# Kernel tuning notes

Hardware: AMD Instinct MI355X
Metric: run time of the kernel (lower is better)

Reference implementation:

```python
import jax, jax.numpy as jnp
import numpy as np

DT_RANK = 128
DIM_INNER = 2048
D_STATE = 16
IN_FEATURES = 2048


def setup_inputs() -> dict:
    key = jax.random.key(0)
    ks = jax.random.split(key, 6)
    B, L = 2, 2048
    x = jax.random.normal(ks[0], (B, L, IN_FEATURES), dtype=jnp.float32)
    out_dbc = DT_RANK + 2 * D_STATE
    W_dbc = jax.random.normal(ks[1], (out_dbc, IN_FEATURES), dtype=jnp.float32) / np.sqrt(IN_FEATURES)
    b_dbc = jax.random.normal(ks[2], (out_dbc,), dtype=jnp.float32) * 0.01
    W_dt = jax.random.normal(ks[3], (DIM_INNER, DT_RANK), dtype=jnp.float32) / np.sqrt(DT_RANK)
    b_dt = jax.random.normal(ks[4], (DIM_INNER,), dtype=jnp.float32) * 0.01
    A_log = jnp.log(jnp.tile(jnp.arange(1, D_STATE + 1, dtype=jnp.float32), (DIM_INNER, 1)))
    D = jnp.ones((DIM_INNER,), dtype=jnp.float32)
    return {"x": x, "W_dbc": W_dbc, "b_dbc": b_dbc, "W_dt": W_dt, "b_dt": b_dt, "A_log": A_log, "D": D}


def _scan_combine(e1, e2):
    a1, b1 = e1
    a2, b2 = e2
    return a1 * a2, a2 * b1 + b2


def reference(x, W_dbc, b_dbc, W_dt, b_dt, A_log, D):
    # x: (B, L, Din) with Din == dim_inner
    A = -jnp.exp(A_log)                               # (Din, N)
    deltaBC = x @ W_dbc.T + b_dbc                     # (B, L, dt_rank + 2N)
    delta_lo = deltaBC[..., :DT_RANK]
    Bmat = deltaBC[..., DT_RANK:DT_RANK + D_STATE]    # (B, L, N)
    Cmat = deltaBC[..., DT_RANK + D_STATE:]           # (B, L, N)
    delta = jax.nn.softplus(delta_lo @ W_dt.T + b_dt) # (B, L, Din)
    deltaA = jnp.exp(delta[..., None] * A)            # (B, L, Din, N)
    BX = (delta[..., None] * Bmat[:, :, None, :]) * x[..., None]  # (B, L, Din, N)
    # first-order linear recurrence h_t = deltaA_t * h_{t-1} + BX_t, h_{-1}=0
    _, hs = jax.lax.associative_scan(_scan_combine, (deltaA, BX), axis=1)
    y = jnp.einsum("blds,bls->bld", hs, Cmat) + D * x
    return y
```

## Files before the change

kernel.cpp:

```cpp
#include <hip/hip_runtime.h>
#include <hip/hip_bf16.h>
#include <math.h>

#define BATCH  2
#define LSEQ   2048
#define FEAT   2048
#define DINNER 2048
#define DSTATE 16
#define DTRANK 128
#define NDBC   160
#define NCHUNK 64
#define LCHUNK (LSEQ / NCHUNK)
#define BL     (BATCH * LSEQ)
#define KSPLIT 4
#define KCH    (FEAT / KSPLIT)
#define KSUB   64
#define BSTRIDE 72

typedef __attribute__((ext_vector_type(8))) short bf16x8;
typedef __attribute__((ext_vector_type(4))) short bf16x4;
typedef __attribute__((ext_vector_type(4))) float floatx4;

#if __has_builtin(__builtin_amdgcn_exp2f)
#define EXP2F(x) __builtin_amdgcn_exp2f(x)
#else
#define EXP2F(x) exp2f(x)
#endif
#if __has_builtin(__builtin_amdgcn_logf)
#define LOG2F(x) __builtin_amdgcn_logf(x)
#else
#define LOG2F(x) __log2f(x)
#endif

__device__ inline float softplus_fast(float v) {
    float e = EXP2F(-fabsf(v) * 1.4426950408889634f);
    return fmaxf(v, 0.f) + 0.6931471805599453f * LOG2F(1.f + e);
}

__device__ inline void split8(floatx4 a0, floatx4 a1, bf16x8* h, bf16x8* l) {
    union { bf16x8 v; __hip_bfloat16 e[8]; } H, L;
    float v[8] = {a0[0], a0[1], a0[2], a0[3], a1[0], a1[1], a1[2], a1[3]};
#pragma unroll
    for (int i = 0; i < 8; ++i) {
        H.e[i] = __float2bfloat16(v[i]);
        L.e[i] = __float2bfloat16(v[i] - __bfloat162float(H.e[i]));
    }
    *h = H.v; *l = L.v;
}

__device__ inline void split_store8(const float* __restrict__ src, int t,
                                    __hip_bfloat16* __restrict__ hi,
                                    __hip_bfloat16* __restrict__ lo) {
    const floatx4* s4 = (const floatx4*)(src) + t * 2;
    bf16x8 h, l;
    split8(s4[0], s4[1], &h, &l);
    ((bf16x8*)hi)[t] = h;
    ((bf16x8*)lo)[t] = l;
}

__global__ __launch_bounds__(256) void prep_all(
    const float* __restrict__ Wdbc, const float* __restrict__ Wdt,
    const float* __restrict__ Alog,
    __hip_bfloat16* __restrict__ wdbch, __hip_bfloat16* __restrict__ wdbcl,
    __hip_bfloat16* __restrict__ wdth, __hip_bfloat16* __restrict__ wdtl,
    float* __restrict__ A2T)
{
    int blk = blockIdx.x;
    if (blk < 160) {
        split_store8(Wdbc, blk * 256 + threadIdx.x, wdbch, wdbcl);
    } else if (blk < 288) {
        split_store8(Wdt, (blk - 160) * 256 + threadIdx.x, wdth, wdtl);
    } else {
        int tid = (blk - 288) * 256 + threadIdx.x;
        int s = tid >> 11;
        int d = tid & (DINNER - 1);
        A2T[s * DINNER + d] = -__expf(Alog[d * DSTATE + s]) * 1.4426950408889634f;
    }
}

__global__ __launch_bounds__(256) void gemm_dbc(
    const float* __restrict__ x,
    const __hip_bfloat16* __restrict__ wh, const __hip_bfloat16* __restrict__ wl,
    float* __restrict__ partial)
{
    __shared__ union {
        struct { __hip_bfloat16 Bh[NDBC * BSTRIDE]; __hip_bfloat16 Bl[NDBC * BSTRIDE]; } s;
        float tile[64 * 164];
    } sm;
    int mt = blockIdx.x, ks = blockIdx.y;
    int t = threadIdx.x;
    int wave = t >> 6, lane = t & 63, lm = lane & 15, q = lane >> 4;
    int m0 = mt * 64;
    int k0 = ks * KCH;
    const float* xrow = x + (size_t)(m0 + wave * 16 + lm) * FEAT;
    floatx4 acc[10];
#pragma unroll
    for (int i = 0; i < 10; ++i) acc[i] = (floatx4){0.f, 0.f, 0.f, 0.f};
    int sr = t >> 3, scb = t & 7;
    for (int kc = 0; kc < KCH; kc += KSUB) {
#pragma unroll
        for (int r = sr; r < NDBC; r += 32) {
            size_t g = (size_t)r * FEAT + k0 + kc + scb * 8;
            *(bf16x8*)&sm.s.Bh[r * BSTRIDE + scb * 8] = *(const bf16x8*)&wh[g];
            *(bf16x8*)&sm.s.Bl[r * BSTRIDE + scb * 8] = *(const bf16x8*)&wl[g];
        }
        __syncthreads();
#pragma unroll
        for (int kk = 0; kk < KSUB; kk += 32) {
            int col = k0 + kc + kk + q * 8;
            floatx4 a0 = *(const floatx4*)(xrow + col);
            floatx4 a1 = *(const floatx4*)(xrow + col + 4);
            bf16x8 ah, al;
            split8(a0, a1, &ah, &al);
#pragma unroll
            for (int nt = 0; nt < 10; ++nt) {
                int boff = (nt * 16 + lm) * BSTRIDE + kk + q * 8;
                bf16x8 bh = *(const bf16x8*)&sm.s.Bh[boff];
                bf16x8 bl = *(const bf16x8*)&sm.s.Bl[boff];
                acc[nt] = __builtin_amdgcn_mfma_f32_16x16x32_bf16(ah, bh, acc[nt], 0, 0, 0);
                acc[nt] = __builtin_amdgcn_mfma_f32_16x16x32_bf16(ah, bl, acc[nt], 0, 0, 0);
                acc[nt] = __builtin_amdgcn_mfma_f32_16x16x32_bf16(al, bh, acc[nt], 0, 0, 0);
            }
        }
        __syncthreads();
    }
#pragma unroll
    for (int nt = 0; nt < 10; ++nt)
#pragma unroll
        for (int i = 0; i < 4; ++i)
            sm.tile[(wave * 16 + q * 4 + i) * 164 + nt * 16 + lm] = acc[nt][i];
    __syncthreads();
#pragma unroll
    for (int it = 0; it < 10; ++it) {
        int idx = it * 256 + t;
        int row = idx / 40, cq = (idx - row * 40) * 4;
        floatx4 v = *(const floatx4*)&sm.tile[row * 164 + cq];
        *(floatx4*)&partial[((size_t)ks * BL + m0 + row) * NDBC + cq] = v;
    }
}

__global__ __launch_bounds__(256) void finalize_dbc(
    const float* __restrict__ partial, const float* __restrict__ bias,
    float* __restrict__ dbcBC, __hip_bfloat16* __restrict__ dhi, __hip_bfloat16* __restrict__ dlo)
{
    int tid = blockIdx.x * 256 + threadIdx.x;
    int m = tid / 40, c4 = tid - m * 40;
    int n = c4 * 4;
    floatx4 s = *(const floatx4*)(bias + n);
#pragma unroll
    for (int ks = 0; ks < KSPLIT; ++ks) {
        floatx4 p = *(const floatx4*)(partial + ((size_t)ks * BL + m) * NDBC + n);
        s = s + p;
    }
    if (c4 < 32) {
        union { bf16x4 v; __hip_bfloat16 e[4]; } H, L;
#pragma unroll
        for (int i = 0; i < 4; ++i) {
            H.e[i] = __float2bfloat16(s[i]);
            L.e[i] = __float2bfloat16(s[i] - __bfloat162float(H.e[i]));
        }
        *(bf16x4*)(dhi + (size_t)m * DTRANK + n) = H.v;
        *(bf16x4*)(dlo + (size_t)m * DTRANK + n) = L.v;
    } else {
        *(floatx4*)(dbcBC + (size_t)m * 32 + (n - 128)) = s;
    }
}

__global__ __launch_bounds__(256) void gemm_dt(
    const __hip_bfloat16* __restrict__ dhi, const __hip_bfloat16* __restrict__ dlo,
    const __hip_bfloat16* __restrict__ wh, const __hip_bfloat16* __restrict__ wl,
    const float* __restrict__ bdt, float* __restrict__ delta)
{
    __shared__ float tile[128 * 68];
    int mt = blockIdx.x, ntb = blockIdx.y;
    int t = threadIdx.x, wave = t >> 6, lane = t & 63, lm = lane & 15, q = lane >> 4;
    int m0 = mt * 128 + wave * 32;
    int n0 = ntb * 64;
    bf16x8 AH[2][4], AL[2][4];
#pragma unroll
    for (int sub = 0; sub < 2; ++sub) {
        const __hip_bfloat16* ah = dhi + (size_t)(m0 + sub * 16 + lm) * DTRANK + q * 8;
        const __hip_bfloat16* al = dlo + (size_t)(m0 + sub * 16 + lm) * DTRANK + q * 8;
#pragma unroll
        for (int kp = 0; kp < 4; ++kp) {
            AH[sub][kp] = *(const bf16x8*)(ah + kp * 32);
            AL[sub][kp] = *(const bf16x8*)(al + kp * 32);
        }
    }
    floatx4 acc[4][2];
#pragma unroll
    for (int i = 0; i < 4; ++i)
#pragma unroll
        for (int j = 0; j < 2; ++j) acc[i][j] = (floatx4){0.f, 0.f, 0.f, 0.f};
#pragma unroll
    for (int nt = 0; nt < 4; ++nt) {
        const __hip_bfloat16* bh = wh + (size_t)(n0 + nt * 16 + lm) * DTRANK + q * 8;
        const __hip_bfloat16* blp = wl + (size_t)(n0 + nt * 16 + lm) * DTRANK + q * 8;
#pragma unroll
        for (int kp = 0; kp < 4; ++kp) {
            bf16x8 bhv = *(const bf16x8*)(bh + kp * 32);
            bf16x8 blv = *(const bf16x8*)(blp + kp * 32);
#pragma unroll
            for (int sub = 0; sub < 2; ++sub) {
                acc[nt][sub] = __builtin_amdgcn_mfma_f32_16x16x32_bf16(AH[sub][kp], bhv, acc[nt][sub], 0, 0, 0);
                acc[nt][sub] = __builtin_amdgcn_mfma_f32_16x16x32_bf16(AH[sub][kp], blv, acc[nt][sub], 0, 0, 0);
                acc[nt][sub] = __builtin_amdgcn_mfma_f32_16x16x32_bf16(AL[sub][kp], bhv, acc[nt][sub], 0, 0, 0);
            }
        }
    }
    int wrow = wave * 32;
#pragma unroll
    for (int nt = 0; nt < 4; ++nt) {
        float bias = bdt[n0 + nt * 16 + lm];
#pragma unroll
        for (int sub = 0; sub < 2; ++sub)
#pragma unroll
            for (int i = 0; i < 4; ++i) {
                float v = acc[nt][sub][i] + bias;
                tile[(wrow + sub * 16 + q * 4 + i) * 68 + nt * 16 + lm] = softplus_fast(v);
            }
    }
    __syncthreads();
#pragma unroll
    for (int it = 0; it < 8; ++it) {
        int idx = it * 256 + t;
        int row = idx >> 4, cq = (idx & 15) * 4;
        floatx4 v = *(const floatx4*)&tile[row * 68 + cq];
        *(floatx4*)&delta[(size_t)(mt * 128 + row) * DINNER + n0 + cq] = v;
    }
}

__global__ __launch_bounds__(256) void scan_partial(
    const float* __restrict__ delta, const float* __restrict__ x,
    const float* __restrict__ dbcBC, const float* __restrict__ A2T,
    float* __restrict__ hA, float* __restrict__ sumd)
{
    __shared__ float BC[LCHUNK * 32];
    int t = threadIdx.x;
    int gtid = blockIdx.x * 256 + t;
    int d = gtid & (DINNER - 1);
    int c = (gtid >> 11) & (NCHUNK - 1);
    int b = gtid >> 17;
    {
        int row = t >> 3, cq = (t & 7) * 4;
        *(floatx4*)&BC[row * 32 + cq] =
            *(const floatx4*)&dbcBC[(size_t)(b * LSEQ + c * LCHUNK + row) * 32 + cq];
    }
    float a2[DSTATE], h[DSTATE];
#pragma unroll
    for (int s = 0; s < DSTATE; ++s) { a2[s] = A2T[s * DINNER + d]; h[s] = 0.f; }
    __syncthreads();
    int base = (b * LSEQ + c * LCHUNK) * DINNER + d;
    const float* dp = delta + base;
    const float* xp = x + base;
    float sd = 0.f;
    auto step = [&](int i, float dl, float xv) {
        float du = dl * xv;
        sd += dl;
        const floatx4* Bq = (const floatx4*)&BC[i * 32];
#pragma unroll
        for (int qq = 0; qq < 4; ++qq) {
            floatx4 Bv = Bq[qq];
#pragma unroll
            for (int j = 0; j < 4; ++j) {
                int s = qq * 4 + j;
                h[s] = fmaf(EXP2F(dl * a2[s]), h[s], du * Bv[j]);
            }
        }
    };
    float dlA = dp[0], xvA = xp[0];
    float dlB = dp[DINNER], xvB = xp[DINNER];
    for (int i = 0; i < LCHUNK - 2; ++i) {
        float dlC = dp[(i + 2) * DINNER];
        float xvC = xp[(i + 2) * DINNER];
        step(i, dlA, xvA);
        dlA = dlB; xvA = xvB; dlB = dlC; xvB = xvC;
    }
    step(LCHUNK - 2, dlA, xvA);
    step(LCHUNK - 1, dlB, xvB);
    size_t hbase = ((size_t)((b * NCHUNK + c) * 4) * DINNER + d) * 4;
#pragma unroll
    for (int qq = 0; qq < 4; ++qq) {
        floatx4 v = {h[qq * 4], h[qq * 4 + 1], h[qq * 4 + 2], h[qq * 4 + 3]};
        *(floatx4*)&hA[hbase + (size_t)qq * DINNER * 4] = v;
    }
    sumd[(size_t)(b * NCHUNK + c) * DINNER + d] = sd;
}

__global__ __launch_bounds__(256) void scan_combine(
    float* __restrict__ hA, const float* __restrict__ sumd, const float* __restrict__ A2T)
{
    int tid = blockIdx.x * 256 + threadIdx.x;
    int s = tid & 15;
    int d = (tid >> 4) & (DINNER - 1);
    int b = tid >> 15;
    float a2s = A2T[s * DINNER + d];
    int q = s >> 2, e = s & 3;
    size_t hoff = ((size_t)(b * NCHUNK * 4 + q) * DINNER + d) * 4 + e;
    size_t soff = (size_t)(b * NCHUNK) * DINNER + d;
    const size_t hstep = (size_t)16 * DINNER;
    float hin = 0.f;
#pragma unroll
    for (int g = 0; g < NCHUNK / 16; ++g) {
        float sdv[16], hv[16];
#pragma unroll
        for (int k = 0; k < 16; ++k) {
            int cc = g * 16 + k;
            sdv[k] = sumd[soff + (size_t)cc * DINNER];
            hv[k] = hA[hoff + (size_t)cc * hstep];
        }
#pragma unroll
        for (int k = 0; k < 16; ++k) {
            int cc = g * 16 + k;
            hA[hoff + (size_t)cc * hstep] = hin;
            hin = EXP2F(a2s * sdv[k]) * hin + hv[k];
        }
    }
}

__global__ __launch_bounds__(256) void scan_final(
    const float* __restrict__ delta, const float* __restrict__ x,
    const float* __restrict__ dbcBC, const float* __restrict__ A2T,
    const float* __restrict__ hin, const float* __restrict__ Dp,
    float* __restrict__ out)
{
    __shared__ float BC[LCHUNK * 32];
    int t = threadIdx.x;
    int gtid = blockIdx.x * 256 + t;
    int d = gtid & (DINNER - 1);
    int c = (gtid >> 11) & (NCHUNK - 1);
    int b = gtid >> 17;
    {
        int row = t >> 3, cq = (t & 7) * 4;
        *(floatx4*)&BC[row * 32 + cq] =
            *(const floatx4*)&dbcBC[(size_t)(b * LSEQ + c * LCHUNK + row) * 32 + cq];
    }
    float a2[DSTATE], h[DSTATE];
    size_t hbase = ((size_t)((b * NCHUNK + c) * 4) * DINNER + d) * 4;
#pragma unroll
    for (int qq = 0; qq < 4; ++qq) {
        floatx4 v = *(const floatx4*)&hin[hbase + (size_t)qq * DINNER * 4];
#pragma unroll
        for (int j = 0; j < 4; ++j) h[qq * 4 + j] = v[j];
    }
#pragma unroll
    for (int s = 0; s < DSTATE; ++s) a2[s] = A2T[s * DINNER + d];
    float Dd = Dp[d];
    __syncthreads();
    int base = (b * LSEQ + c * LCHUNK) * DINNER + d;
    const float* dp = delta + base;
    const float* xp = x + base;
    float* op = out + base;
    auto step = [&](int i, float dl, float xv) {
        float du = dl * xv;
        float y = 0.f;
        const floatx4* Pq = (const floatx4*)&BC[i * 32];
#pragma unroll
        for (int qq = 0; qq < 4; ++qq) {
            floatx4 Bv = Pq[qq];
            floatx4 Cv = Pq[qq + 4];
#pragma unroll
            for (int j = 0; j < 4; ++j) {
                int s = qq * 4 + j;
                h[s] = fmaf(EXP2F(dl * a2[s]), h[s], du * Bv[j]);
                y = fmaf(h[s], Cv[j], y);
            }
        }
        op[i * DINNER] = fmaf(Dd, xv, y);
    };
    float dlA = dp[0], xvA = xp[0];
    float dlB = dp[DINNER], xvB = xp[DINNER];
    for (int i = 0; i < LCHUNK - 2; ++i) {
        float dlC = dp[(i + 2) * DINNER];
        float xvC = xp[(i + 2) * DINNER];
        step(i, dlA, xvA);
        dlA = dlB; xvA = xvB; dlB = dlC; xvB = xvC;
    }
    step(LCHUNK - 2, dlA, xvA);
    step(LCHUNK - 1, dlB, xvB);
}

extern "C" void kernel_launch(void* const* d_in, const int* in_sizes, int n_in,
                              void* d_out, int out_size, void* d_ws, size_t ws_size,
                              hipStream_t stream) {
    const float* x    = (const float*)d_in[0];
    const float* Wdbc = (const float*)d_in[1];
    const float* bdbc = (const float*)d_in[2];
    const float* Wdt  = (const float*)d_in[3];
    const float* bdt  = (const float*)d_in[4];
    const float* Alog = (const float*)d_in[5];
    const float* Dp   = (const float*)d_in[6];
    float* out = (float*)d_out;

    char* w = (char*)d_ws;
    __hip_bfloat16* wdbch = (__hip_bfloat16*)w;  w += (size_t)NDBC * FEAT * 2;
    __hip_bfloat16* wdbcl = (__hip_bfloat16*)w;  w += (size_t)NDBC * FEAT * 2;
    __hip_bfloat16* wdth = (__hip_bfloat16*)w;   w += (size_t)DINNER * DTRANK * 2;
    __hip_bfloat16* wdtl = (__hip_bfloat16*)w;   w += (size_t)DINNER * DTRANK * 2;
    float* partial = (float*)w;                  w += (size_t)KSPLIT * BL * NDBC * 4;
    float* dbcBC = (float*)w;                    w += (size_t)BL * 32 * 4;
    __hip_bfloat16* dhi = (__hip_bfloat16*)w;    w += (size_t)BL * DTRANK * 2;
    __hip_bfloat16* dlo = (__hip_bfloat16*)w;    w += (size_t)BL * DTRANK * 2;
    float* delta = (float*)w;                    w += (size_t)BL * DINNER * 4;
    float* A2T = (float*)w;                      w += (size_t)DSTATE * DINNER * 4;
    float* hA = (float*)w;                       w += (size_t)BATCH * NCHUNK * DINNER * DSTATE * 4;
    float* sumd = (float*)w;                     w += (size_t)BATCH * NCHUNK * DINNER * 4;

    hipLaunchKernelGGL(prep_all, dim3(416), dim3(256), 0, stream,
                       Wdbc, Wdt, Alog, wdbch, wdbcl, wdth, wdtl, A2T);
    hipLaunchKernelGGL(gemm_dbc, dim3(BL / 64, KSPLIT), dim3(256), 0, stream,
                       x, wdbch, wdbcl, partial);
    hipLaunchKernelGGL(finalize_dbc, dim3(BL * 40 / 256), dim3(256), 0, stream,
                       partial, bdbc, dbcBC, dhi, dlo);
    hipLaunchKernelGGL(gemm_dt, dim3(BL / 128, DINNER / 64), dim3(256), 0, stream,
                       dhi, dlo, wdth, wdtl, bdt, delta);
    hipLaunchKernelGGL(scan_partial, dim3((BATCH * NCHUNK * DINNER) / 256), dim3(256), 0, stream,
                       delta, x, dbcBC, A2T, hA, sumd);
    hipLaunchKernelGGL(scan_combine, dim3((BATCH * DINNER * DSTATE) / 256), dim3(256), 0, stream,
                       hA, sumd, A2T);
    hipLaunchKernelGGL(scan_final, dim3((BATCH * NCHUNK * DINNER) / 256), dim3(256), 0, stream,
                       delta, x, dbcBC, A2T, hA, Dp, out);
}
```

Baseline: 210.5 us.

## Batch-prefetch scan inputs in groups of eight and double K-split of projection GEMM

```diff
diff --git a/kernel.cpp b/kernel.cpp
--- a/kernel.cpp
+++ b/kernel.cpp
@@ -12,10 +12,11 @@
 #define NCHUNK 64
 #define LCHUNK (LSEQ / NCHUNK)
 #define BL     (BATCH * LSEQ)
-#define KSPLIT 4
+#define KSPLIT 8
 #define KCH    (FEAT / KSPLIT)
 #define KSUB   64
 #define BSTRIDE 72
+#define GRP    8
 
 typedef __attribute__((ext_vector_type(8))) short bf16x8;
 typedef __attribute__((ext_vector_type(4))) short bf16x4;
@@ -254,30 +255,36 @@
     const float* dp = delta + base;
     const float* xp = x + base;
     float sd = 0.f;
-    auto step = [&](int i, float dl, float xv) {
-        float du = dl * xv;
-        sd += dl;
-        const floatx4* Bq = (const floatx4*)&BC[i * 32];
-#pragma unroll
-        for (int qq = 0; qq < 4; ++qq) {
-            floatx4 Bv = Bq[qq];
-#pragma unroll
-            for (int j = 0; j < 4; ++j) {
-                int s = qq * 4 + j;
-                h[s] = fmaf(EXP2F(dl * a2[s]), h[s], du * Bv[j]);
-            }
-        }
-    };
-    float dlA = dp[0], xvA = xp[0];
-    float dlB = dp[DINNER], xvB = xp[DINNER];
-    for (int i = 0; i < LCHUNK - 2; ++i) {
-        float dlC = dp[(i + 2) * DINNER];
-        float xvC = xp[(i + 2) * DINNER];
-        step(i, dlA, xvA);
-        dlA = dlB; xvA = xvB; dlB = dlC; xvB = xvC;
-    }
-    step(LCHUNK - 2, dlA, xvA);
-    step(LCHUNK - 1, dlB, xvB);
+    float dlb[2][GRP], xvb[2][GRP];
+#pragma unroll
+    for (int j = 0; j < GRP; ++j) { dlb[0][j] = dp[j * DINNER]; xvb[0][j] = xp[j * DINNER]; }
+#pragma unroll
+    for (int g = 0; g < LCHUNK / GRP; ++g) {
+        int p = g & 1;
+        if (g + 1 < LCHUNK / GRP) {
+#pragma unroll
+            for (int j = 0; j < GRP; ++j) {
+                dlb[1 - p][j] = dp[((g + 1) * GRP + j) * DINNER];
+                xvb[1 - p][j] = xp[((g + 1) * GRP + j) * DINNER];
+            }
+        }
+#pragma unroll
+        for (int j = 0; j < GRP; ++j) {
+            float dl = dlb[p][j], xv = xvb[p][j];
+            float du = dl * xv;
+            sd += dl;
+            const floatx4* Bq = (const floatx4*)&BC[(g * GRP + j) * 32];
+#pragma unroll
+            for (int qq = 0; qq < 4; ++qq) {
+                floatx4 Bv = Bq[qq];
+#pragma unroll
+                for (int jj = 0; jj < 4; ++jj) {
+                    int s = qq * 4 + jj;
+                    h[s] = fmaf(EXP2F(dl * a2[s]), h[s], du * Bv[jj]);
+                }
+            }
+        }
+    }
     size_t hbase = ((size_t)((b * NCHUNK + c) * 4) * DINNER + d) * 4;
 #pragma unroll
     for (int qq = 0; qq < 4; ++qq) {
@@ -351,33 +358,40 @@
     const float* dp = delta + base;
     const float* xp = x + base;
     float* op = out + base;
-    auto step = [&](int i, float dl, float xv) {
-        float du = dl * xv;
-        float y = 0.f;
-        const floatx4* Pq = (const floatx4*)&BC[i * 32];
-#pragma unroll
-        for (int qq = 0; qq < 4; ++qq) {
-            floatx4 Bv = Pq[qq];
-            floatx4 Cv = Pq[qq + 4];
-#pragma unroll
-            for (int j = 0; j < 4; ++j) {
-                int s = qq * 4 + j;
-                h[s] = fmaf(EXP2F(dl * a2[s]), h[s], du * Bv[j]);
-                y = fmaf(h[s], Cv[j], y);
-            }
-        }
-        op[i * DINNER] = fmaf(Dd, xv, y);
-    };
-    float dlA = dp[0], xvA = xp[0];
-    float dlB = dp[DINNER], xvB = xp[DINNER];
-    for (int i = 0; i < LCHUNK - 2; ++i) {
-        float dlC = dp[(i + 2) * DINNER];
-        float xvC = xp[(i + 2) * DINNER];
-        step(i, dlA, xvA);
-        dlA = dlB; xvA = xvB; dlB = dlC; xvB = xvC;
-    }
-    step(LCHUNK - 2, dlA, xvA);
-    step(LCHUNK - 1, dlB, xvB);
+    float dlb[2][GRP], xvb[2][GRP];
+#pragma unroll
+    for (int j = 0; j < GRP; ++j) { dlb[0][j] = dp[j * DINNER]; xvb[0][j] = xp[j * DINNER]; }
+#pragma unroll
+    for (int g = 0; g < LCHUNK / GRP; ++g) {
+        int p = g & 1;
+        if (g + 1 < LCHUNK / GRP) {
+#pragma unroll
+            for (int j = 0; j < GRP; ++j) {
+                dlb[1 - p][j] = dp[((g + 1) * GRP + j) * DINNER];
+                xvb[1 - p][j] = xp[((g + 1) * GRP + j) * DINNER];
+            }
+        }
+#pragma unroll
+        for (int j = 0; j < GRP; ++j) {
+            float dl = dlb[p][j], xv = xvb[p][j];
+            int i = g * GRP + j;
+            float du = dl * xv;
+            float y = 0.f;
+            const floatx4* Pq = (const floatx4*)&BC[i * 32];
+#pragma unroll
+            for (int qq = 0; qq < 4; ++qq) {
+                floatx4 Bv = Pq[qq];
+                floatx4 Cv = Pq[qq + 4];
+#pragma unroll
+                for (int jj = 0; jj < 4; ++jj) {
+                    int s = qq * 4 + jj;
+                    h[s] = fmaf(EXP2F(dl * a2[s]), h[s], du * Bv[jj]);
+                    y = fmaf(h[s], Cv[jj], y);
+                }
+            }
+            op[i * DINNER] = fmaf(Dd, xv, y);
+        }
+    }
 }
 
 extern "C" void kernel_launch(void* const* d_in, const int* in_sizes, int n_in,
```

After: 206.2 us. 2.1% less time.
